# Performance work log

Measured on AMD Instinct MI355X. Metric: run time of the kernel, lower is better.

Reference implementation:

```python
import jax, jax.numpy as jnp
import numpy as np

EPS = 1e-6
NUM_HEADS = 24

def _rmsnorm(x, w):
    # x: [..., D], fp32 math as in FluxRMSNorm
    xf = x.astype(jnp.float32)
    inv = jax.lax.rsqrt(jnp.mean(xf * xf, axis=-1, keepdims=True) + EPS)
    return w * (xf * inv).astype(x.dtype)

def setup_inputs() -> dict:
    key = jax.random.key(0)
    ks = jax.random.split(key, 4)
    B, N, H = 1, 2048, 3072
    D = H // NUM_HEADS
    s_in = 1.0 / np.sqrt(H)
    return {
        "x": jax.random.normal(ks[0], (B, N, H), jnp.float32),
        "Wqkv": jax.random.normal(ks[1], (H, 3 * H), jnp.float32) * s_in,
        "b_qkv": jnp.zeros((3 * H,), jnp.float32),
        "Wproj": jax.random.normal(ks[2], (H, H), jnp.float32) * s_in,
        "q_norm_w": jnp.ones((D,), jnp.float32),
        "k_norm_w": jnp.ones((D,), jnp.float32),
    }

def reference(x, Wqkv, b_qkv, Wproj, q_norm_w, k_norm_w):
    B, N, hidden = x.shape
    nh = NUM_HEADS
    hd = hidden // nh
    scale = hd ** (-0.5)
    qkv = (x @ Wqkv + b_qkv).reshape(B, N, 3, nh, hd)
    q, k, v = qkv[:, :, 0], qkv[:, :, 1], qkv[:, :, 2]  # [B,N,nh,hd]
    q = _rmsnorm(q, q_norm_w)
    k = _rmsnorm(k, k_norm_w)
    # scores: [B,nh,N,N]
    scores = jnp.einsum('bqhd,bkhd->bhqk', q, k) * scale
    attn = jax.nn.softmax(scores, axis=-1)
    out = jnp.einsum('bhqk,bkhd->bqhd', attn, v).reshape(B, N, hidden)
    return out @ Wproj
```

## Files before the change

kernel.cpp:

```cpp
#include <hip/hip_runtime.h>
#include <hip/hip_bf16.h>

using bf16 = __hip_bfloat16;
typedef __attribute__((ext_vector_type(8))) short short8;
typedef __attribute__((ext_vector_type(4))) float f32x4;
typedef unsigned long long ull;

static constexpr int SEQ  = 2048;
static constexpr int HID  = 3072;
static constexpr int NH   = 24;
static constexpr int HD   = 128;
static constexpr int QKVN = 9216;

__device__ __forceinline__ f32x4 mfma_16x16x32(short8 a, short8 b, f32x4 c) {
  return __builtin_amdgcn_mfma_f32_16x16x32_bf16(a, b, c, 0, 0, 0);
}

#define GLOAD_LDS16(g, l) __builtin_amdgcn_global_load_lds(                 \
    (const __attribute__((address_space(1))) void*)(g),                    \
    (__attribute__((address_space(3))) void*)(l), 16, 0, 0)

typedef __attribute__((address_space(3))) const unsigned char lds_cchar;

__device__ __forceinline__ unsigned pack_bf16(float lo, float hi) {
  bf16 l = __float2bfloat16(lo), h = __float2bfloat16(hi);
  return (unsigned)*(unsigned short*)&l | ((unsigned)*(unsigned short*)&h << 16);
}

__global__ __launch_bounds__(256)
void cvt_f32_bf16_vec(const float* __restrict__ src, bf16* __restrict__ dst, int n4) {
  int i = blockIdx.x * 256 + threadIdx.x;
  if (i >= n4) return;
  float4 v = ((const float4*)src)[i];
  ushort4 o;
  bf16 t0 = __float2bfloat16(v.x); o.x = *(unsigned short*)&t0;
  bf16 t1 = __float2bfloat16(v.y); o.y = *(unsigned short*)&t1;
  bf16 t2 = __float2bfloat16(v.z); o.z = *(unsigned short*)&t2;
  bf16 t3 = __float2bfloat16(v.w); o.w = *(unsigned short*)&t3;
  ((ushort4*)dst)[i] = o;
}

__global__ __launch_bounds__(256)
void transpose_cvt64(const float* __restrict__ src, bf16* __restrict__ dst, int R, int C) {
  __shared__ float tile[32][65];
  const int c0 = blockIdx.x * 64, r0 = blockIdx.y * 32;
  const int lc = threadIdx.x & 63, lt = threadIdx.x >> 6;
  #pragma unroll
  for (int i = 0; i < 8; ++i)
    tile[lt + i * 4][lc] = src[(size_t)(r0 + lt + i * 4) * C + c0 + lc];
  __syncthreads();
  const int u = threadIdx.x & 15, dr = threadIdx.x >> 4;
  #pragma unroll
  for (int j = 0; j < 4; ++j) {
    const int cc = dr + j * 16;
    bf16 x0 = __float2bfloat16(tile[u * 2][cc]);
    bf16 x1 = __float2bfloat16(tile[u * 2 + 1][cc]);
    ushort2 o;
    o.x = *(unsigned short*)&x0; o.y = *(unsigned short*)&x1;
    *(ushort2*)&dst[(size_t)(c0 + cc) * R + r0 + u * 2] = o;
  }
}

template<int BIAS>
__global__ __launch_bounds__(768, 3)
void gemm12w(const bf16* __restrict__ A, const bf16* __restrict__ BT,
             const float* __restrict__ bias, bf16* __restrict__ Cout,
             int M, int N, int K) {
  __shared__ __align__(16) bf16 Asb[2][256 * 64];
  __shared__ __align__(16) bf16 Bsb[2][288 * 64];

  const int tid  = threadIdx.x;
  const int lane = tid & 63;
  const int wid  = tid >> 6;
  const int wmm  = wid & 3;
  const int wnn  = wid >> 2;
  const int lr   = lane & 15;
  const int lg   = lane >> 4;

  const int xcd = blockIdx.x & 7;
  const int q   = blockIdx.x >> 3;
  const int bm  = (q & 7) * 256;
  const int bn  = (xcd * 4 + (q >> 3)) * 288;

  const int lrow = lane >> 3;
  const int csrc = ((lane & 7) ^ lrow) * 8;
  const bf16* Abase = A  + (size_t)(bm + lrow) * K + csrc;
  const bf16* Bbase = BT + (size_t)(bn + lrow) * K + csrc;

#define STG12(b, u, i) do {                                                       \
    const int L_ = wid + 12 * (i);                                                \
    if (L_ < 32)      GLOAD_LDS16(Abase + (size_t)(8 * L_) * K + (size_t)(u) * 64,\
                                  &Asb[b][L_ * 512]);                             \
    else if (L_ < 68) GLOAD_LDS16(Bbase + (size_t)(8 * (L_ - 32)) * K + (size_t)(u) * 64, \
                                  &Bsb[b][(L_ - 32) * 512]);                      \
  } while (0)
#define RA12(b, m, kk) (*(const short8*)(&Asb[b][(wmm * 64 + (m) * 16 + lr) * 64 \
                          + ((((kk) * 4 + lg)) ^ (lr & 7)) * 8]))
#define RB12(b, n, kk) (*(const short8*)(&Bsb[b][(wnn * 96 + (n) * 16 + lr) * 64 \
                          + ((((kk) * 4 + lg)) ^ (lr & 7)) * 8]))

  f32x4 acc[4][6] = {};
  const int NT = K >> 6;

  #pragma unroll
  for (int i = 0; i < 6; ++i) STG12(0, 0, i);

  for (int t = 0; t < NT; ++t) {
    const int c = t & 1, nc = c ^ 1;
    const bool pf = (t + 1) < NT;
    short8 a[4], b[6];

    asm volatile("s_waitcnt vmcnt(0)" ::: "memory");
    __builtin_amdgcn_s_barrier();

    if (pf) {
      STG12(nc, t + 1, 0); STG12(nc, t + 1, 1); STG12(nc, t + 1, 2);
      STG12(nc, t + 1, 3); STG12(nc, t + 1, 4); STG12(nc, t + 1, 5);
    }
    __builtin_amdgcn_sched_barrier(0);

    b[0] = RB12(c, 0, 0); b[1] = RB12(c, 1, 0); b[2] = RB12(c, 2, 0);
    b[3] = RB12(c, 3, 0); b[4] = RB12(c, 4, 0); b[5] = RB12(c, 5, 0);
    a[0] = RA12(c, 0, 0); a[1] = RA12(c, 1, 0); a[2] = RA12(c, 2, 0); a[3] = RA12(c, 3, 0);
    #pragma unroll
    for (int n = 0; n < 6; ++n)
      #pragma unroll
      for (int m = 0; m < 4; ++m) acc[m][n] = mfma_16x16x32(a[m], b[n], acc[m][n]);

    b[0] = RB12(c, 0, 1); b[1] = RB12(c, 1, 1); b[2] = RB12(c, 2, 1);
    b[3] = RB12(c, 3, 1); b[4] = RB12(c, 4, 1); b[5] = RB12(c, 5, 1);
    a[0] = RA12(c, 0, 1); a[1] = RA12(c, 1, 1); a[2] = RA12(c, 2, 1); a[3] = RA12(c, 3, 1);
    #pragma unroll
    for (int n = 0; n < 6; ++n)
      #pragma unroll
      for (int m = 0; m < 4; ++m) acc[m][n] = mfma_16x16x32(a[m], b[n], acc[m][n]);
  }
#undef STG12
#undef RA12
#undef RB12

  const int row0 = bm + wmm * 64 + lg * 4;
  const int col0 = bn + wnn * 96 + lr;
  #pragma unroll
  for (int n = 0; n < 6; ++n) {
    const int col = col0 + n * 16;
    const float bv = BIAS ? bias[col] : 0.0f;
    #pragma unroll
    for (int m = 0; m < 4; ++m)
      #pragma unroll
      for (int r = 0; r < 4; ++r)
        Cout[(size_t)(row0 + m * 16 + r) * N + col] = __float2bfloat16(acc[m][n][r] + bv);
  }
}

__global__ __launch_bounds__(256, 2)
void gemm4w(const bf16* __restrict__ A, const bf16* __restrict__ BT,
            float* __restrict__ Cout, int M, int N, int K) {
  __shared__ __align__(16) bf16 Asb[2][128 * 64];
  __shared__ __align__(16) bf16 Bsb[2][96 * 64];

  const int tid  = threadIdx.x;
  const int lane = tid & 63;
  const int wid  = tid >> 6;
  const int wm   = wid >> 1;
  const int wn   = wid & 1;
  const int lr   = lane & 15;
  const int lg   = lane >> 4;

  const int xcd = blockIdx.x & 7;
  const int q   = blockIdx.x >> 3;
  const int bm  = (q & 15) * 128;
  const int bn  = (xcd * 4 + (q >> 4)) * 96;

  const int lrow = lane >> 3;
  const int csrc = ((lane & 7) ^ lrow) * 8;
  const bf16* Abase = A  + (size_t)(bm + lrow) * K + csrc;
  const bf16* Bbase = BT + (size_t)(bn + lrow) * K + csrc;

#define STG4(b, u, i) do {                                                        \
    const int L_ = wid + 4 * (i);                                                 \
    if (L_ < 16)      GLOAD_LDS16(Abase + (size_t)(8 * L_) * K + (size_t)(u) * 64,\
                                  &Asb[b][L_ * 512]);                             \
    else if (L_ < 28) GLOAD_LDS16(Bbase + (size_t)(8 * (L_ - 16)) * K + (size_t)(u) * 64, \
                                  &Bsb[b][(L_ - 16) * 512]);                      \
  } while (0)
#define RA4(b, m, kk) (*(const short8*)(&Asb[b][(wm * 64 + (m) * 16 + lr) * 64 \
                          + ((((kk) * 4 + lg)) ^ (lr & 7)) * 8]))
#define RB4(b, n, kk) (*(const short8*)(&Bsb[b][(wn * 48 + (n) * 16 + lr) * 64 \
                          + ((((kk) * 4 + lg)) ^ (lr & 7)) * 8]))

  f32x4 acc[4][3] = {};
  const int NT = K >> 6;

  #pragma unroll
  for (int i = 0; i < 7; ++i) STG4(0, 0, i);

  for (int t = 0; t < NT; ++t) {
    const int c = t & 1, nc = c ^ 1;
    const bool pf = (t + 1) < NT;
    short8 a[4], b[3];

    asm volatile("s_waitcnt vmcnt(0)" ::: "memory");
    __builtin_amdgcn_s_barrier();

    if (pf) {
      STG4(nc, t + 1, 0); STG4(nc, t + 1, 1); STG4(nc, t + 1, 2); STG4(nc, t + 1, 3);
      STG4(nc, t + 1, 4); STG4(nc, t + 1, 5); STG4(nc, t + 1, 6);
    }
    __builtin_amdgcn_sched_barrier(0);

    b[0] = RB4(c, 0, 0); b[1] = RB4(c, 1, 0); b[2] = RB4(c, 2, 0);
    a[0] = RA4(c, 0, 0); a[1] = RA4(c, 1, 0); a[2] = RA4(c, 2, 0); a[3] = RA4(c, 3, 0);
    #pragma unroll
    for (int n = 0; n < 3; ++n)
      #pragma unroll
      for (int m = 0; m < 4; ++m) acc[m][n] = mfma_16x16x32(a[m], b[n], acc[m][n]);

    b[0] = RB4(c, 0, 1); b[1] = RB4(c, 1, 1); b[2] = RB4(c, 2, 1);
    a[0] = RA4(c, 0, 1); a[1] = RA4(c, 1, 1); a[2] = RA4(c, 2, 1); a[3] = RA4(c, 3, 1);
    #pragma unroll
    for (int n = 0; n < 3; ++n)
      #pragma unroll
      for (int m = 0; m < 4; ++m) acc[m][n] = mfma_16x16x32(a[m], b[n], acc[m][n]);
  }
#undef STG4
#undef RA4
#undef RB4

  const int row0 = bm + wm * 64 + lg * 4;
  const int col0 = bn + wn * 48 + lr;
  #pragma unroll
  for (int n = 0; n < 3; ++n) {
    const int col = col0 + n * 16;
    #pragma unroll
    for (int m = 0; m < 4; ++m)
      #pragma unroll
      for (int r = 0; r < 4; ++r)
        Cout[(size_t)(row0 + m * 16 + r) * N + col] = acc[m][n][r];
  }
}

__global__ __launch_bounds__(256)
void rmsnorm_qk(bf16* __restrict__ qkv, const float* __restrict__ qw,
                const float* __restrict__ kw) {
  const int row  = blockIdx.x * 4 + (threadIdx.x >> 6);
  const int lane = threadIdx.x & 63;
  const int token = row / 48;
  const int rem   = row - token * 48;
  const int which = rem / 24;
  const int head  = rem - which * 24;
  bf16* p = qkv + (size_t)token * QKVN + which * HID + head * HD;
  const float a = __bfloat162float(p[lane * 2]);
  const float b = __bfloat162float(p[lane * 2 + 1]);
  float ss = a * a + b * b;
  #pragma unroll
  for (int mask = 32; mask >= 1; mask >>= 1) ss += __shfl_xor(ss, mask);
  const float inv = rsqrtf(ss * (1.0f / 128.0f) + 1e-6f);
  const float* w = which ? kw : qw;
  p[lane * 2]     = __float2bfloat16(a * inv * w[lane * 2]);
  p[lane * 2 + 1] = __float2bfloat16(b * inv * w[lane * 2 + 1]);
}

__global__ __launch_bounds__(256, 3)
void attn_kernel(const bf16* __restrict__ qkv, bf16* __restrict__ ctx) {
  const int head = blockIdx.y;
  const int qb   = blockIdx.x;
  const int tid  = threadIdx.x;
  const int lane = tid & 63;
  const int wid  = tid >> 6;
  const int lr   = lane & 15;
  const int lg   = lane >> 4;

  __shared__ __align__(16) unsigned char Ksb[64 * 256];
  __shared__ __align__(16) unsigned char Vsb[128 * 128];
  __shared__ __align__(16) unsigned short Ps[4][16 * 72];

  const int qrow0 = qb * 64 + wid * 16;
  short8 qf[4];
  #pragma unroll
  for (int kt = 0; kt < 4; ++kt)
    qf[kt] = *(const short8*)(qkv + (size_t)(qrow0 + lr) * QKVN + head * HD + kt * 32 + lg * 8);

  f32x4 oacc[8] = {};
  float mrun = -1e30f, lsum = 0.0f;

  const float scale = 0.088388347648318447f;

  const int stok = tid >> 4;
  const int sdc  = tid & 15;

  short8 kreg[4], vreg[4];
  #pragma unroll
  for (int j = 0; j < 4; ++j) {
    const int tok = stok + (j & 1) * 16 + (j >> 1) * 32;
    kreg[j] = *(const short8*)(qkv + (size_t)tok * QKVN + HID     + head * HD + sdc * 8);
    vreg[j] = *(const short8*)(qkv + (size_t)tok * QKVN + 2 * HID + head * HD + sdc * 8);
  }

#define TRISSUE(S, dtv) {                                                         \
    lds_cchar* pd_ = vb0 + (dtv) * 2048;                                          \
    asm volatile("ds_read_b64_tr_b16 %0, %1 offset:0"    : "=v"(S##0) : "v"(pd_));\
    asm volatile("ds_read_b64_tr_b16 %0, %1 offset:512"  : "=v"(S##1) : "v"(pd_));\
    asm volatile("ds_read_b64_tr_b16 %0, %1 offset:1024" : "=v"(S##2) : "v"(pd_));\
    asm volatile("ds_read_b64_tr_b16 %0, %1 offset:1536" : "=v"(S##3) : "v"(pd_));}
#define TRMFMA(S, dtv) {                                                          \
    short8 v0_, v1_;                                                              \
    ((ull*)&v0_)[0] = S##0; ((ull*)&v0_)[1] = S##1;                               \
    ((ull*)&v1_)[0] = S##2; ((ull*)&v1_)[1] = S##3;                               \
    oacc[dtv] = mfma_16x16x32(pa[0], v0_, oacc[dtv]);                             \
    oacc[dtv] = mfma_16x16x32(pa[1], v1_, oacc[dtv]); }
#define TRWAIT4 asm volatile("s_waitcnt lgkmcnt(4)" ::: "memory"); \
                __builtin_amdgcn_sched_barrier(0);

  for (int t = 0; t < SEQ / 64; ++t) {
    __syncthreads();
    #pragma unroll
    for (int j = 0; j < 4; ++j) {
      const int tok = stok + (j & 1) * 16 + (j >> 1) * 32;
      const int dc  = sdc;
      *(short8*)(Ksb + ((tok * 256 + dc * 16) ^ ((tok & 7) << 4))) = kreg[j];
      const int dg = dc >> 1, h = dc & 1, kg = tok >> 2, kr = tok & 3;
      const int pos = (kg & 8) | ((kg & 1) << 2) | ((kg >> 1) & 3);
      *(short8*)(Vsb + (dg * 16 + pos) * 128 + kr * 32 + h * 16) = vreg[j];
    }
    __syncthreads();

    if (t + 1 < SEQ / 64) {
      const int kv1 = (t + 1) * 64;
      #pragma unroll
      for (int j = 0; j < 4; ++j) {
        const int tok = kv1 + stok + (j & 1) * 16 + (j >> 1) * 32;
        kreg[j] = *(const short8*)(qkv + (size_t)tok * QKVN + HID     + head * HD + sdc * 8);
        vreg[j] = *(const short8*)(qkv + (size_t)tok * QKVN + 2 * HID + head * HD + sdc * 8);
      }
      __builtin_amdgcn_sched_barrier(0);
    }

    f32x4 st[4];
    __builtin_amdgcn_s_setprio(1);
    #pragma unroll
    for (int ct = 0; ct < 4; ++ct) {
      f32x4 a = {};
      #pragma unroll
      for (int kt = 0; kt < 4; ++kt) {
        short8 kb = *(const short8*)(Ksb +
            ((((ct * 16 + lr) * 256) + kt * 64 + lg * 16) ^ ((lr & 7) << 4)));
        a = mfma_16x16x32(kb, qf[kt], a);
      }
      st[ct] = a;
    }
    __builtin_amdgcn_s_setprio(0);

    float pm = st[0][0];
    #pragma unroll
    for (int ct = 0; ct < 4; ++ct)
      #pragma unroll
      for (int r = 0; r < 4; ++r) pm = fmaxf(pm, st[ct][r]);
    pm *= scale;
    pm = fmaxf(pm, __shfl_xor(pm, 16));
    pm = fmaxf(pm, __shfl_xor(pm, 32));

    if (!__all(pm <= mrun + 8.0f)) {
      const float mnew = fmaxf(mrun, pm);
      const float corr = __expf(mrun - mnew);
      mrun = mnew;
      lsum *= corr;
      #pragma unroll
      for (int r = 0; r < 4; ++r) {
        const float cr = __shfl(corr, lg * 4 + r);
        #pragma unroll
        for (int dt = 0; dt < 8; ++dt) oacc[dt][r] *= cr;
      }
    }

    float ps = 0.0f;
    #pragma unroll
    for (int ct = 0; ct < 4; ++ct) {
      const float p0 = __expf(st[ct][0] * scale - mrun);
      const float p1 = __expf(st[ct][1] * scale - mrun);
      const float p2 = __expf(st[ct][2] * scale - mrun);
      const float p3 = __expf(st[ct][3] * scale - mrun);
      ps += (p0 + p1) + (p2 + p3);
      uint2 w;
      w.x = pack_bf16(p0, p1);
      w.y = pack_bf16(p2, p3);
      *(uint2*)&Ps[wid][lr * 72 + ct * 16 + lg * 4] = w;
    }
    lsum += ps;

    short8 pa[2];
    pa[0] = *(const short8*)&Ps[wid][lr * 72 + lg * 8];
    pa[1] = *(const short8*)&Ps[wid][lr * 72 + 32 + lg * 8];
    __builtin_amdgcn_sched_barrier(0);

    lds_cchar* vb0 = (lds_cchar*)Vsb + lane * 8;
    ull x0, x1, x2, x3, y0, y1, y2, y3;
    __builtin_amdgcn_s_setprio(1);
    TRISSUE(x, 0)
    TRISSUE(y, 1)
    TRWAIT4  TRMFMA(x, 0)  TRISSUE(x, 2)
    TRWAIT4  TRMFMA(y, 1)  TRISSUE(y, 3)
    TRWAIT4  TRMFMA(x, 2)  TRISSUE(x, 4)
    TRWAIT4  TRMFMA(y, 3)  TRISSUE(y, 5)
    TRWAIT4  TRMFMA(x, 4)  TRISSUE(x, 6)
    TRWAIT4  TRMFMA(y, 5)  TRISSUE(y, 7)
    TRWAIT4  TRMFMA(x, 6)
    asm volatile("s_waitcnt lgkmcnt(0)" ::: "memory");
    __builtin_amdgcn_sched_barrier(0);
    TRMFMA(y, 7)
    __builtin_amdgcn_s_setprio(0);
  }
#undef TRISSUE
#undef TRMFMA
#undef TRWAIT4

  lsum += __shfl_xor(lsum, 16);
  lsum += __shfl_xor(lsum, 32);
  const float invl = 1.0f / lsum;
  #pragma unroll
  for (int r = 0; r < 4; ++r) {
    const float inv = __shfl(invl, lg * 4 + r);
    const size_t tok = qrow0 + lg * 4 + r;
    #pragma unroll
    for (int dt = 0; dt < 8; ++dt)
      ctx[tok * HID + head * HD + dt * 16 + lr] = __float2bfloat16(oacc[dt][r] * inv);
  }
}

extern "C" void kernel_launch(void* const* d_in, const int* in_sizes, int n_in,
                              void* d_out, int out_size, void* d_ws, size_t ws_size,
                              hipStream_t stream) {
  (void)in_sizes; (void)n_in; (void)out_size; (void)ws_size;
  const float* x     = (const float*)d_in[0];
  const float* Wqkv  = (const float*)d_in[1];
  const float* bqkv  = (const float*)d_in[2];
  const float* Wproj = (const float*)d_in[3];
  const float* qw    = (const float*)d_in[4];
  const float* kw    = (const float*)d_in[5];

  char* ws = (char*)d_ws;
  bf16* xb     = (bf16*)ws;
  bf16* WqkvT  = (bf16*)(ws + 12582912);
  bf16* WprojT = (bf16*)(ws + 69206016);
  bf16* qkv    = (bf16*)(ws + 88080384);
  bf16* ctx    = xb;

  cvt_f32_bf16_vec<<<(SEQ * HID / 4 + 255) / 256, 256, 0, stream>>>(x, xb, SEQ * HID / 4);
  transpose_cvt64<<<dim3(QKVN / 64, HID / 32), 256, 0, stream>>>(Wqkv, WqkvT, HID, QKVN);
  transpose_cvt64<<<dim3(HID / 64, HID / 32), 256, 0, stream>>>(Wproj, WprojT, HID, HID);

  gemm12w<1><<<256, 768, 0, stream>>>(xb, WqkvT, bqkv, qkv, SEQ, QKVN, HID);

  rmsnorm_qk<<<SEQ * 48 / 4, 256, 0, stream>>>(qkv, qw, kw);

  attn_kernel<<<dim3(SEQ / 64, NH), 256, 0, stream>>>(qkv, ctx);

  gemm4w<<<512, 256, 0, stream>>>(ctx, WprojT, (float*)d_out, SEQ, HID, HID);
}
```

Measured before the change: 310.7 us.

## Process 32 query rows per wave in attention with 2-wave blocks

The attention kernel now runs two waves per block, each handling 32 query rows as two 16-row halves. Every K fragment read from LDS and every V transpose read now feeds two MFMAs, which halves LDS read traffic per unit of compute. The cost is twice the accumulator and Q registers per wave, fewer waves per block to hide latency, and eight K/V staging loads per thread instead of four.

```diff
diff --git a/kernel.cpp b/kernel.cpp
--- a/kernel.cpp
+++ b/kernel.cpp
@@ -261,7 +261,7 @@
   p[lane * 2 + 1] = __float2bfloat16(b * inv * w[lane * 2 + 1]);
 }
 
-__global__ __launch_bounds__(256, 3)
+__global__ __launch_bounds__(128)
 void attn_kernel(const bf16* __restrict__ qkv, bf16* __restrict__ ctx) {
   const int head = blockIdx.y;
   const int qb   = blockIdx.x;
@@ -273,26 +273,29 @@
 
   __shared__ __align__(16) unsigned char Ksb[64 * 256];
   __shared__ __align__(16) unsigned char Vsb[128 * 128];
-  __shared__ __align__(16) unsigned short Ps[4][16 * 72];
-
-  const int qrow0 = qb * 64 + wid * 16;
-  short8 qf[4];
-  #pragma unroll
-  for (int kt = 0; kt < 4; ++kt)
-    qf[kt] = *(const short8*)(qkv + (size_t)(qrow0 + lr) * QKVN + head * HD + kt * 32 + lg * 8);
-
-  f32x4 oacc[8] = {};
-  float mrun = -1e30f, lsum = 0.0f;
+  __shared__ __align__(16) unsigned short Ps[2][32 * 72];
+
+  const int qrow0 = qb * 64 + wid * 32;
+  short8 qf0[4], qf1[4];
+  #pragma unroll
+  for (int kt = 0; kt < 4; ++kt) {
+    qf0[kt] = *(const short8*)(qkv + (size_t)(qrow0 + lr) * QKVN + head * HD + kt * 32 + lg * 8);
+    qf1[kt] = *(const short8*)(qkv + (size_t)(qrow0 + 16 + lr) * QKVN + head * HD + kt * 32 + lg * 8);
+  }
+
+  f32x4 oacc0[8] = {}, oacc1[8] = {};
+  float mrun0 = -1e30f, lsum0 = 0.0f;
+  float mrun1 = -1e30f, lsum1 = 0.0f;
 
   const float scale = 0.088388347648318447f;
 
   const int stok = tid >> 4;
   const int sdc  = tid & 15;
 
-  short8 kreg[4], vreg[4];
-  #pragma unroll
-  for (int j = 0; j < 4; ++j) {
-    const int tok = stok + (j & 1) * 16 + (j >> 1) * 32;
+  short8 kreg[8], vreg[8];
+  #pragma unroll
+  for (int j = 0; j < 8; ++j) {
+    const int tok = stok + j * 8;
     kreg[j] = *(const short8*)(qkv + (size_t)tok * QKVN + HID     + head * HD + sdc * 8);
     vreg[j] = *(const short8*)(qkv + (size_t)tok * QKVN + 2 * HID + head * HD + sdc * 8);
   }
@@ -307,16 +310,18 @@
     short8 v0_, v1_;                                                              \
     ((ull*)&v0_)[0] = S##0; ((ull*)&v0_)[1] = S##1;                               \
     ((ull*)&v1_)[0] = S##2; ((ull*)&v1_)[1] = S##3;                               \
-    oacc[dtv] = mfma_16x16x32(pa[0], v0_, oacc[dtv]);                             \
-    oacc[dtv] = mfma_16x16x32(pa[1], v1_, oacc[dtv]); }
+    oacc0[dtv] = mfma_16x16x32(pa00, v0_, oacc0[dtv]);                            \
+    oacc0[dtv] = mfma_16x16x32(pa01, v1_, oacc0[dtv]);                            \
+    oacc1[dtv] = mfma_16x16x32(pa10, v0_, oacc1[dtv]);                            \
+    oacc1[dtv] = mfma_16x16x32(pa11, v1_, oacc1[dtv]); }
 #define TRWAIT4 asm volatile("s_waitcnt lgkmcnt(4)" ::: "memory"); \
                 __builtin_amdgcn_sched_barrier(0);
 
   for (int t = 0; t < SEQ / 64; ++t) {
     __syncthreads();
     #pragma unroll
-    for (int j = 0; j < 4; ++j) {
-      const int tok = stok + (j & 1) * 16 + (j >> 1) * 32;
+    for (int j = 0; j < 8; ++j) {
+      const int tok = stok + j * 8;
       const int dc  = sdc;
       *(short8*)(Ksb + ((tok * 256 + dc * 16) ^ ((tok & 7) << 4))) = kreg[j];
       const int dg = dc >> 1, h = dc & 1, kg = tok >> 2, kr = tok & 3;
@@ -328,69 +333,75 @@
     if (t + 1 < SEQ / 64) {
       const int kv1 = (t + 1) * 64;
       #pragma unroll
-      for (int j = 0; j < 4; ++j) {
-        const int tok = kv1 + stok + (j & 1) * 16 + (j >> 1) * 32;
+      for (int j = 0; j < 8; ++j) {
+        const int tok = kv1 + stok + j * 8;
         kreg[j] = *(const short8*)(qkv + (size_t)tok * QKVN + HID     + head * HD + sdc * 8);
         vreg[j] = *(const short8*)(qkv + (size_t)tok * QKVN + 2 * HID + head * HD + sdc * 8);
       }
       __builtin_amdgcn_sched_barrier(0);
     }
 
-    f32x4 st[4];
+    f32x4 st0[4], st1[4];
     __builtin_amdgcn_s_setprio(1);
     #pragma unroll
     for (int ct = 0; ct < 4; ++ct) {
-      f32x4 a = {};
+      f32x4 a0 = {}, a1 = {};
       #pragma unroll
       for (int kt = 0; kt < 4; ++kt) {
         short8 kb = *(const short8*)(Ksb +
             ((((ct * 16 + lr) * 256) + kt * 64 + lg * 16) ^ ((lr & 7) << 4)));
-        a = mfma_16x16x32(kb, qf[kt], a);
+        a0 = mfma_16x16x32(kb, qf0[kt], a0);
+        a1 = mfma_16x16x32(kb, qf1[kt], a1);
       }
-      st[ct] = a;
+      st0[ct] = a0; st1[ct] = a1;
     }
     __builtin_amdgcn_s_setprio(0);
 
-    float pm = st[0][0];
-    #pragma unroll
-    for (int ct = 0; ct < 4; ++ct)
-      #pragma unroll
-      for (int r = 0; r < 4; ++r) pm = fmaxf(pm, st[ct][r]);
-    pm *= scale;
-    pm = fmaxf(pm, __shfl_xor(pm, 16));
-    pm = fmaxf(pm, __shfl_xor(pm, 32));
-
-    if (!__all(pm <= mrun + 8.0f)) {
-      const float mnew = fmaxf(mrun, pm);
-      const float corr = __expf(mrun - mnew);
-      mrun = mnew;
-      lsum *= corr;
-      #pragma unroll
-      for (int r = 0; r < 4; ++r) {
-        const float cr = __shfl(corr, lg * 4 + r);
-        #pragma unroll
-        for (int dt = 0; dt < 8; ++dt) oacc[dt][r] *= cr;
-      }
-    }
-
-    float ps = 0.0f;
-    #pragma unroll
-    for (int ct = 0; ct < 4; ++ct) {
-      const float p0 = __expf(st[ct][0] * scale - mrun);
-      const float p1 = __expf(st[ct][1] * scale - mrun);
-      const float p2 = __expf(st[ct][2] * scale - mrun);
-      const float p3 = __expf(st[ct][3] * scale - mrun);
-      ps += (p0 + p1) + (p2 + p3);
-      uint2 w;
-      w.x = pack_bf16(p0, p1);
-      w.y = pack_bf16(p2, p3);
-      *(uint2*)&Ps[wid][lr * 72 + ct * 16 + lg * 4] = w;
-    }
-    lsum += ps;
-
-    short8 pa[2];
-    pa[0] = *(const short8*)&Ps[wid][lr * 72 + lg * 8];
-    pa[1] = *(const short8*)&Ps[wid][lr * 72 + 32 + lg * 8];
+#define SOFTMAX_HALF(ST, MR, LS, OACC, ROWB)  {                                   \
+    float pm = ST[0][0];                                                          \
+    _Pragma("unroll")                                                             \
+    for (int ct = 0; ct < 4; ++ct)                                                \
+      _Pragma("unroll")                                                           \
+      for (int r = 0; r < 4; ++r) pm = fmaxf(pm, ST[ct][r]);                      \
+    pm *= scale;                                                                  \
+    pm = fmaxf(pm, __shfl_xor(pm, 16));                                           \
+    pm = fmaxf(pm, __shfl_xor(pm, 32));                                           \
+    if (!__all(pm <= MR + 8.0f)) {                                                \
+      const float mnew = fmaxf(MR, pm);                                           \
+      const float corr = __expf(MR - mnew);                                       \
+      MR = mnew;                                                                  \
+      LS *= corr;                                                                 \
+      _Pragma("unroll")                                                           \
+      for (int r = 0; r < 4; ++r) {                                               \
+        const float cr = __shfl(corr, lg * 4 + r);                                \
+        _Pragma("unroll")                                                         \
+        for (int dt = 0; dt < 8; ++dt) OACC[dt][r] *= cr;                         \
+      }                                                                           \
+    }                                                                             \
+    float ps = 0.0f;                                                              \
+    _Pragma("unroll")                                                             \
+    for (int ct = 0; ct < 4; ++ct) {                                              \
+      const float p0 = __expf(ST[ct][0] * scale - MR);                            \
+      const float p1 = __expf(ST[ct][1] * scale - MR);                            \
+      const float p2 = __expf(ST[ct][2] * scale - MR);                            \
+      const float p3 = __expf(ST[ct][3] * scale - MR);                            \
+      ps += (p0 + p1) + (p2 + p3);                                                \
+      uint2 w;                                                                    \
+      w.x = pack_bf16(p0, p1);                                                    \
+      w.y = pack_bf16(p2, p3);                                                    \
+      *(uint2*)&Ps[wid][(ROWB + lr) * 72 + ct * 16 + lg * 4] = w;                 \
+    }                                                                             \
+    LS += ps; }
+
+    SOFTMAX_HALF(st0, mrun0, lsum0, oacc0, 0)
+    SOFTMAX_HALF(st1, mrun1, lsum1, oacc1, 16)
+#undef SOFTMAX_HALF
+
+    short8 pa00, pa01, pa10, pa11;
+    pa00 = *(const short8*)&Ps[wid][lr * 72 + lg * 8];
+    pa01 = *(const short8*)&Ps[wid][lr * 72 + 32 + lg * 8];
+    pa10 = *(const short8*)&Ps[wid][(16 + lr) * 72 + lg * 8];
+    pa11 = *(const short8*)&Ps[wid][(16 + lr) * 72 + 32 + lg * 8];
     __builtin_amdgcn_sched_barrier(0);
 
     lds_cchar* vb0 = (lds_cchar*)Vsb + lane * 8;
@@ -414,16 +425,23 @@
 #undef TRMFMA
 #undef TRWAIT4
 
-  lsum += __shfl_xor(lsum, 16);
-  lsum += __shfl_xor(lsum, 32);
-  const float invl = 1.0f / lsum;
+  lsum0 += __shfl_xor(lsum0, 16);
+  lsum0 += __shfl_xor(lsum0, 32);
+  lsum1 += __shfl_xor(lsum1, 16);
+  lsum1 += __shfl_xor(lsum1, 32);
+  const float invl0 = 1.0f / lsum0;
+  const float invl1 = 1.0f / lsum1;
   #pragma unroll
   for (int r = 0; r < 4; ++r) {
-    const float inv = __shfl(invl, lg * 4 + r);
-    const size_t tok = qrow0 + lg * 4 + r;
-    #pragma unroll
-    for (int dt = 0; dt < 8; ++dt)
-      ctx[tok * HID + head * HD + dt * 16 + lr] = __float2bfloat16(oacc[dt][r] * inv);
+    const float i0 = __shfl(invl0, lg * 4 + r);
+    const float i1 = __shfl(invl1, lg * 4 + r);
+    const size_t tok0 = qrow0 + lg * 4 + r;
+    const size_t tok1 = qrow0 + 16 + lg * 4 + r;
+    #pragma unroll
+    for (int dt = 0; dt < 8; ++dt) {
+      ctx[tok0 * HID + head * HD + dt * 16 + lr] = __float2bfloat16(oacc0[dt][r] * i0);
+      ctx[tok1 * HID + head * HD + dt * 16 + lr] = __float2bfloat16(oacc1[dt][r] * i1);
+    }
   }
 }
 
@@ -453,7 +471,7 @@
 
   rmsnorm_qk<<<SEQ * 48 / 4, 256, 0, stream>>>(qkv, qw, kw);
 
-  attn_kernel<<<dim3(SEQ / 64, NH), 256, 0, stream>>>(qkv, ctx);
+  attn_kernel<<<dim3(SEQ / 64, NH), 128, 0, stream>>>(qkv, ctx);
 
   gemm4w<<<512, 256, 0, stream>>>(ctx, WprojT, (float*)d_out, SEQ, HID, HID);
 }
```

Measured after the change: 378.2 us. 1.22x slower.
